# Performance work log

Measured on AMD Instinct MI355X. Metric: run time of the kernel, lower is better.

## Reference

```python
import jax, jax.numpy as jnp
import numpy as np

H = 128          # GRU hidden size (fixed in module)
EPS = 1e-8       # torch CosineSimilarity eps


def _gru_dir(x, w_ih, w_hh, b_ih, b_hh, reverse):
    # x: [B, L, D]; torch GRU gate math, single direction
    B = x.shape[0]
    gx = jnp.einsum('bld,gd->blg', x, w_ih) + b_ih  # [B, L, 3H]

    def step(h, gx_t):
        gh = h @ w_hh.T + b_hh
        xr, xz, xn = jnp.split(gx_t, 3, axis=-1)
        hr, hz, hn = jnp.split(gh, 3, axis=-1)
        r = jax.nn.sigmoid(xr + hr)
        z = jax.nn.sigmoid(xz + hz)
        n = jnp.tanh(xn + r * hn)
        h_new = (1.0 - z) * n + z * h
        return h_new, h_new

    h0 = jnp.zeros((B, H), x.dtype)
    h_last, outs = jax.lax.scan(step, h0, jnp.swapaxes(gx, 0, 1), reverse=reverse)
    return jnp.swapaxes(outs, 0, 1), h_last  # [B, L, H], [B, H]


def _bigru(x, p):
    # p = (w_ih_f, w_hh_f, b_ih_f, b_hh_f, w_ih_b, w_hh_b, b_ih_b, b_hh_b)
    of, hf = _gru_dir(x, p[0], p[1], p[2], p[3], False)
    ob, hb = _gru_dir(x, p[4], p[5], p[6], p[7], True)
    # outs concat = torch bidirectional output; [hf, hb] concat == h_n.transpose(1,0).reshape(B,-1)
    return jnp.concatenate([of, ob], axis=-1), jnp.concatenate([hf, hb], axis=-1)


def _cosnorm(x):
    return x / jnp.maximum(jnp.linalg.norm(x, axis=-1, keepdims=True), EPS)


def _forward(context, options, rnn_p, attn_p):
    ctx_outs, ctx_h = _bigru(context, rnn_p)  # [B, L1, 2H], [B, 2H]

    def per_option(option):  # option: [B, L2, D]
        opt_outs, _ = _bigru(option, rnn_p)  # [B, L2, 2H]
        # cosine-similarity attention == matmul of L2-normalized vectors
        # (replaces the original O(B*L2*L1*2H) repeated tensors, same math)
        att = jnp.einsum('bqh,bkh->bqk', _cosnorm(opt_outs), _cosnorm(ctx_outs))  # [B, L2, L1]
        att = jax.nn.softmax(att, axis=2)  # softmax over context positions (dim=2)
        att_opt = jnp.einsum('bqk,bkh->bqh', att, ctx_outs)  # bmm -> [B, L2, 2H]
        cat = jnp.concatenate([att_opt, opt_outs], axis=-1)  # [B, L2, 4H]
        _, ao_h = _bigru(cat, attn_p)  # [B, 2H]
        num = jnp.sum(ctx_h * ao_h, axis=-1)
        den = jnp.maximum(jnp.linalg.norm(ctx_h, axis=-1), EPS) * \
              jnp.maximum(jnp.linalg.norm(ao_h, axis=-1), EPS)
        return num / den  # [B]

    logits = jax.vmap(per_option)(jnp.swapaxes(options, 0, 1))  # [N, B]
    return jax.nn.softmax(logits.T, axis=1)  # [B, N]


def setup_inputs():
    key = jax.random.key(0)
    ks = jax.random.split(key, 24)
    B, L1, L2, N, D = 64, 512, 50, 10, 300
    inp = {
        'context': jax.random.normal(ks[0], (B, L1, D), jnp.float32),
        'context_lens': jax.random.randint(ks[1], (B,), 1, L1),
        'options': jax.random.normal(ks[2], (B, N, L2, D), jnp.float32),
        'option_lens': jax.random.randint(ks[3], (B, N), 1, L2),
    }
    names = ['rw_ih_f', 'rw_hh_f', 'rb_ih_f', 'rb_hh_f',
             'rw_ih_b', 'rw_hh_b', 'rb_ih_b', 'rb_hh_b',
             'aw_ih_f', 'aw_hh_f', 'ab_ih_f', 'ab_hh_f',
             'aw_ih_b', 'aw_hh_b', 'ab_ih_b', 'ab_hh_b']
    shapes = [(3 * H, D), (3 * H, H), (3 * H,), (3 * H,)] * 2 + \
             [(3 * H, 4 * H), (3 * H, H), (3 * H,), (3 * H,)] * 2
    for i, (n, sh) in enumerate(zip(names, shapes)):
        inp[n] = jax.random.normal(ks[4 + i], sh, jnp.float32) * 0.05
    return inp


def reference(context, context_lens, options, option_lens,
              rw_ih_f, rw_hh_f, rb_ih_f, rb_hh_f,
              rw_ih_b, rw_hh_b, rb_ih_b, rb_hh_b,
              aw_ih_f, aw_hh_f, ab_ih_f, ab_hh_f,
              aw_ih_b, aw_hh_b, ab_ih_b, ab_hh_b):
    rnn_p = (rw_ih_f, rw_hh_f, rb_ih_f, rb_hh_f, rw_ih_b, rw_hh_b, rb_ih_b, rb_hh_b)
    attn_p = (aw_ih_f, aw_hh_f, ab_ih_f, ab_hh_f, aw_ih_b, aw_hh_b, ab_ih_b, ab_hh_b)
    return _forward(context, options, rnn_p, attn_p)
```

## Files before the change

### kernel.cpp

```cpp
#include <hip/hip_runtime.h>
#include <math.h>

#define EPS 1e-8f

typedef _Float16 h2_t __attribute__((ext_vector_type(2)));
typedef _Float16 half8 __attribute__((ext_vector_type(8)));
typedef float f32x4 __attribute__((ext_vector_type(4)));

__device__ __forceinline__ float fsig(float x)  { return 1.0f / (1.0f + __expf(-x)); }
__device__ __forceinline__ float ftanh(float x) { return 1.0f - 2.0f / (1.0f + __expf(2.0f * x)); }

__global__ __launch_bounds__(256) void prep_w_k(
    const float* __restrict__ rwf, const float* __restrict__ rwb,
    const float* __restrict__ awf, const float* __restrict__ awb,
    const float* __restrict__ rbf, const float* __restrict__ rbb,
    const float* __restrict__ abf, const float* __restrict__ abb,
    const float* __restrict__ rhf, const float* __restrict__ rhb,
    const float* __restrict__ ahf, const float* __restrict__ ahb,
    _Float16* __restrict__ wrh, _Float16* __restrict__ wah,
    _Float16* __restrict__ wr16, _Float16* __restrict__ wa16,
    float* __restrict__ br, float* __restrict__ ba)
{
    int idx = blockIdx.x * 256 + threadIdx.x;
    if (idx < 768 * 320) {
        int g = idx / 320, k = idx % 320;
        float v = 0.f;
        if (k < 300) v = (g < 384) ? rwf[g * 300 + k] : rwb[(g - 384) * 300 + k];
        wrh[idx] = (_Float16)v;
    }
    if (idx < 768 * 512) {
        int g = idx / 512, k = idx % 512;
        wah[idx] = (_Float16)((g < 384) ? awf[g * 512 + k] : awb[(g - 384) * 512 + k]);
    }
    if (idx < 2 * 384 * 128) {
        int d = idx / 49152, r = idx % 49152;
        wr16[idx] = (_Float16)(d ? rhb[r] : rhf[r]);
        wa16[idx] = (_Float16)(d ? ahb[r] : ahf[r]);
    }
    if (idx < 768) {
        br[idx] = (idx < 384) ? rbf[idx] : rbb[idx - 384];
        ba[idx] = (idx < 384) ? abf[idx] : abb[idx - 384];
    }
}

__global__ __launch_bounds__(256) void conv_k(
    const float* __restrict__ ctx, const float* __restrict__ opt,
    _Float16* __restrict__ ctxh, _Float16* __restrict__ opth)
{
    int idx = blockIdx.x * 256 + threadIdx.x;
    if (idx < 32768 * 320) {
        int r = idx / 320, k = idx % 320;
        ctxh[idx] = (k < 300) ? (_Float16)ctx[r * 300 + k] : (_Float16)0.f;
    }
    if (idx < 32000 * 320) {
        int r = idx / 320, k = idx % 320;
        opth[idx] = (k < 300) ? (_Float16)opt[r * 300 + k] : (_Float16)0.f;
    }
}

template <bool TRBS, bool SPLITA, bool HASBIAS>
__global__ __launch_bounds__(256, 4) void hgemm_k(
    const _Float16* __restrict__ A, const _Float16* __restrict__ A2,
    const _Float16* __restrict__ B, const float* __restrict__ bias,
    _Float16* __restrict__ C, int M, int N, int K,
    int lda, int ldb, int ldc, long sA, long sB, int bdiv, long sC)
{
    const int jn = blockIdx.x * 64;
    const int im = blockIdx.y * 64;
    const int z  = blockIdx.z;
    const _Float16* Bb = B + (size_t)(z / bdiv) * sB;
    _Float16* Cb = C + (size_t)z * sC;

    __shared__ __align__(16) _Float16 As[64 * 64];
    __shared__ __align__(16) _Float16 Bs[64 * 64];

    const int tid  = threadIdx.x;
    const int arow = tid >> 2;
    const int akof = (tid & 3) * 8;
    const int lane = tid & 63;
    const int wv   = tid >> 6;
    const int wm   = (wv & 1) * 32;
    const int wn   = (wv >> 1) * 32;
    const int fm   = lane & 15;
    const int quad = lane >> 4;

    f32x4 acc[2][2];
#pragma unroll
    for (int a = 0; a < 2; a++)
#pragma unroll
        for (int b = 0; b < 2; b++) acc[a][b] = (f32x4)0.f;

    for (int k0 = 0; k0 < K; k0 += 64) {
        {
            const int row = im + arow;
#pragma unroll
            for (int hh = 0; hh < 2; hh++) {
                half8 av = (half8)(_Float16)0.f;
                const int kg = k0 + akof + 32 * hh;
                if (row < M) {
                    if constexpr (SPLITA) {
                        const _Float16* Ah  = A + (size_t)z * sA;
                        const _Float16* A2h = A2 + (size_t)z * sA;
                        const _Float16* ap = (kg < 256)
                            ? (Ah + (size_t)row * lda + kg)
                            : (A2h + (size_t)row * lda + (kg - 256));
                        av = *(const half8*)ap;
                    } else {
                        av = *(const half8*)(A + (size_t)z * sA + (size_t)row * lda + kg);
                    }
                }
                *(half8*)&As[arow * 64 + akof + 32 * hh] = av;
            }
        }
        if constexpr (!TRBS) {
#pragma unroll
            for (int hh = 0; hh < 2; hh++) {
                half8 bv = *(const half8*)(Bb + (size_t)(jn + arow) * ldb
                                           + k0 + akof + 32 * hh);
                *(half8*)&Bs[arow * 64 + akof + 32 * hh] = bv;
            }
        } else {
            const int kk = tid >> 3, noff = (tid & 7) * 8;
            half8 bv0 = *(const half8*)(Bb + (size_t)(k0 + kk) * ldb + jn + noff);
            half8 bv1 = *(const half8*)(Bb + (size_t)(k0 + kk + 32) * ldb + jn + noff);
#pragma unroll
            for (int e = 0; e < 8; e++) {
                Bs[(noff + e) * 64 + kk]      = bv0[e];
                Bs[(noff + e) * 64 + kk + 32] = bv1[e];
            }
        }
        __syncthreads();

        const _Float16* Asp = As + (wm + fm) * 64 + quad * 8;
        const _Float16* Bsp = Bs + (wn + fm) * 64 + quad * 8;
#pragma unroll
        for (int kh = 0; kh < 64; kh += 32) {
            half8 a0 = *(const half8*)(Asp + kh);
            half8 a1 = *(const half8*)(Asp + 16 * 64 + kh);
            half8 b0 = *(const half8*)(Bsp + kh);
            half8 b1 = *(const half8*)(Bsp + 16 * 64 + kh);
            acc[0][0] = __builtin_amdgcn_mfma_f32_16x16x32_f16(a0, b0, acc[0][0], 0, 0, 0);
            acc[0][1] = __builtin_amdgcn_mfma_f32_16x16x32_f16(a0, b1, acc[0][1], 0, 0, 0);
            acc[1][0] = __builtin_amdgcn_mfma_f32_16x16x32_f16(a1, b0, acc[1][0], 0, 0, 0);
            acc[1][1] = __builtin_amdgcn_mfma_f32_16x16x32_f16(a1, b1, acc[1][1], 0, 0, 0);
        }
        __syncthreads();
    }

#pragma unroll
    for (int tm = 0; tm < 2; tm++) {
#pragma unroll
        for (int tn = 0; tn < 2; tn++) {
            const int col  = jn + wn + tn * 16 + fm;
            const int row0 = im + wm + tm * 16 + quad * 4;
            const float bv = HASBIAS ? bias[col] : 0.f;
#pragma unroll
            for (int r = 0; r < 4; r++) {
                const int row = row0 + r;
                if (row < M)
                    Cb[(size_t)row * ldc + col] = (_Float16)(acc[tm][tn][r] + bv);
            }
        }
    }
}

__global__ __launch_bounds__(512, 2) void gru_rec_k(
    const _Float16* __restrict__ gx,
    const _Float16* __restrict__ whh16,
    const float* __restrict__ bhh_f, const float* __restrict__ bhh_b,
    _Float16* __restrict__ outs_h, float* __restrict__ hfin, int L)
{
    const int dir = blockIdx.x & 1;
    const int s   = blockIdx.x >> 1;
    const int t   = threadIdx.x;
    const int w   = t >> 6;
    const int l   = t & 63;
    const int i   = w * 16 + (l & 15);
    const int kq  = l >> 4;
    const _Float16* Wd = whh16 + (size_t)dir * 49152;
    const float* bh = dir ? bhh_b : bhh_f;

    h2_t w2[3][16];
#pragma unroll
    for (int j = 0; j < 3; j++) {
        const _Float16* Wr = Wd + (size_t)(i + 128 * j) * 128 + 32 * kq;
#pragma unroll
        for (int q = 0; q < 16; q++)
            w2[j][q] = *(const h2_t*)(Wr + 2 * q);
    }
    const float b0 = bh[i], b1 = bh[i + 128], b2 = bh[i + 256];

    __shared__ __align__(16) _Float16 h1[2][128];
    __shared__ __align__(16) _Float16 gxs[64][384];
    __shared__ __align__(16) _Float16 outb[64][128];
    if (t < 128) h1[0][t] = (_Float16)0.f;
    float hprev = 0.f;

    for (int t0 = 0; t0 < L; t0 += 64) {
        const int Tc = (L - t0 < 64) ? (L - t0) : 64;
#pragma unroll
        for (int r = 0; r < 6; r++) {
            const int q = t + 512 * r;
            if (q < Tc * 48) {
                const int j = q / 48, off = (q % 48) * 8;
                const int tt = dir ? (L - 1 - (t0 + j)) : (t0 + j);
                *(half8*)&gxs[j][off] =
                    *(const half8*)(gx + ((size_t)s * L + tt) * 768 + dir * 384 + off);
            }
        }
        __syncthreads();

        for (int j = 0; j < Tc; j++) {
            const int cb = (t0 + j) & 1;
            const h2_t* hp = (const h2_t*)&h1[cb][32 * kq];
            float a0 = 0.f, a1 = 0.f, a2 = 0.f;
#pragma unroll
            for (int q = 0; q < 16; q++) {
                h2_t hq = hp[q];
                a0 = __builtin_amdgcn_fdot2(w2[0][q], hq, a0, false);
                a1 = __builtin_amdgcn_fdot2(w2[1][q], hq, a1, false);
                a2 = __builtin_amdgcn_fdot2(w2[2][q], hq, a2, false);
            }
            a0 += __shfl_xor(a0, 16); a0 += __shfl_xor(a0, 32);
            a1 += __shfl_xor(a1, 16); a1 += __shfl_xor(a1, 32);
            a2 += __shfl_xor(a2, 16); a2 += __shfl_xor(a2, 32);
            const float xc0 = (float)gxs[j][i];
            const float xc1 = (float)gxs[j][i + 128];
            const float xc2 = (float)gxs[j][i + 256];
            const float r  = fsig(xc0 + a0 + b0);
            const float zz = fsig(xc1 + a1 + b1);
            const float n  = ftanh(xc2 + r * (a2 + b2));
            const float hnew = (1.0f - zz) * n + zz * hprev;
            hprev = hnew;
            if (kq == 0) {
                h1[cb ^ 1][i] = (_Float16)hnew;
                outb[j][i]    = (_Float16)hnew;
            }
            __syncthreads();
        }

        if (outs_h) {
#pragma unroll
            for (int r = 0; r < 2; r++) {
                const int q = t + 512 * r;
                if (q < Tc * 16) {
                    const int j = q / 16, off = (q % 16) * 8;
                    const int tt = dir ? (L - 1 - (t0 + j)) : (t0 + j);
                    *(half8*)(outs_h + ((size_t)s * L + tt) * 256 + dir * 128 + off) =
                        *(const half8*)&outb[j][off];
                }
            }
        }
    }
    if (hfin && kq == 0) hfin[(size_t)s * 256 + dir * 128 + i] = hprev;
}

__global__ __launch_bounds__(256) void rowinv_k(const _Float16* __restrict__ x,
                                                float* __restrict__ rinv)
{
    const int row = blockIdx.x;
    float v = (float)x[(size_t)row * 256 + threadIdx.x];
    float ss = v * v;
#pragma unroll
    for (int o = 32; o > 0; o >>= 1) ss += __shfl_down(ss, o);
    __shared__ float ps[4];
    if ((threadIdx.x & 63) == 0) ps[threadIdx.x >> 6] = ss;
    __syncthreads();
    if (threadIdx.x == 0)
        rinv[row] = 1.0f / fmaxf(sqrtf(ps[0] + ps[1] + ps[2] + ps[3]), EPS);
}

__global__ __launch_bounds__(256) void att_softmax_k(
    _Float16* __restrict__ att, const float* __restrict__ rinv_opt_l,
    const float* __restrict__ rinv_ctx, int sbase)
{
    const int row = blockIdx.x;
    const int b = (sbase + row / 50) / 10;
    _Float16* p = att + (size_t)row * 512;
    const float* rc = rinv_ctx + b * 512;
    const float sA = rinv_opt_l[row];
    const int t = threadIdx.x;

    float v0 = (float)p[t]       * (sA * rc[t]);
    float v1 = (float)p[t + 256] * (sA * rc[t + 256]);

    __shared__ float red[4];
    float m = fmaxf(v0, v1);
#pragma unroll
    for (int o = 32; o > 0; o >>= 1) m = fmaxf(m, __shfl_down(m, o));
    if ((t & 63) == 0) red[t >> 6] = m;
    __syncthreads();
    m = fmaxf(fmaxf(red[0], red[1]), fmaxf(red[2], red[3]));
    float e0 = __expf(v0 - m), e1 = __expf(v1 - m);
    float ssum = e0 + e1;
#pragma unroll
    for (int o = 32; o > 0; o >>= 1) ssum += __shfl_down(ssum, o);
    __syncthreads();
    if ((t & 63) == 0) red[t >> 6] = ssum;
    __syncthreads();
    float inv = 1.0f / (red[0] + red[1] + red[2] + red[3]);
    p[t]       = (_Float16)(e0 * inv);
    p[t + 256] = (_Float16)(e1 * inv);
}

__global__ __launch_bounds__(256) void logits_k(const float* __restrict__ ch,
                                                const float* __restrict__ ah,
                                                float* __restrict__ logits)
{
    const int s = blockIdx.x;
    const int b = s / 10;
    const int t = threadIdx.x;
    float a = ch[b * 256 + t];
    float c = ah[(size_t)s * 256 + t];
    float num = a * c, na = a * a, nc = c * c;
#pragma unroll
    for (int o = 32; o > 0; o >>= 1) {
        num += __shfl_down(num, o);
        na  += __shfl_down(na,  o);
        nc  += __shfl_down(nc,  o);
    }
    __shared__ float pn[4], pa[4], pc[4];
    if ((t & 63) == 0) { pn[t >> 6] = num; pa[t >> 6] = na; pc[t >> 6] = nc; }
    __syncthreads();
    if (t == 0) {
        float sn = pn[0] + pn[1] + pn[2] + pn[3];
        float sa = pa[0] + pa[1] + pa[2] + pa[3];
        float sc = pc[0] + pc[1] + pc[2] + pc[3];
        logits[s] = sn / (fmaxf(sqrtf(sa), EPS) * fmaxf(sqrtf(sc), EPS));
    }
}

__global__ __launch_bounds__(64) void soft10_k(const float* __restrict__ logits,
                                               float* __restrict__ out)
{
    const int b = blockIdx.x;
    const int t = threadIdx.x;
    __shared__ float v[10];
    if (t < 10) v[t] = logits[b * 10 + t];
    __syncthreads();
    if (t < 10) {
        float m = v[0];
#pragma unroll
        for (int i = 1; i < 10; i++) m = fmaxf(m, v[i]);
        float ssum = 0.f;
#pragma unroll
        for (int i = 0; i < 10; i++) ssum += __expf(v[i] - m);
        out[b * 10 + t] = __expf(v[t] - m) / ssum;
    }
}

extern "C" void kernel_launch(void* const* d_in, const int* in_sizes, int n_in,
                              void* d_out, int out_size, void* d_ws, size_t ws_size,
                              hipStream_t stream)
{
    const float* context = (const float*)d_in[0];
    const float* options = (const float*)d_in[2];
    const float* rw_ih_f = (const float*)d_in[4];
    const float* rw_hh_f = (const float*)d_in[5];
    const float* rb_ih_f = (const float*)d_in[6];
    const float* rb_hh_f = (const float*)d_in[7];
    const float* rw_ih_b = (const float*)d_in[8];
    const float* rw_hh_b = (const float*)d_in[9];
    const float* rb_ih_b = (const float*)d_in[10];
    const float* rb_hh_b = (const float*)d_in[11];
    const float* aw_ih_f = (const float*)d_in[12];
    const float* aw_hh_f = (const float*)d_in[13];
    const float* ab_ih_f = (const float*)d_in[14];
    const float* ab_hh_f = (const float*)d_in[15];
    const float* aw_ih_b = (const float*)d_in[16];
    const float* aw_hh_b = (const float*)d_in[17];
    const float* ab_ih_b = (const float*)d_in[18];
    const float* ab_hh_b = (const float*)d_in[19];

    const size_t persist = 15222144;
    static const int cands[6][2] = {{1,2},{1,4},{2,4},{2,8},{4,16},{8,16}};
    int CC = 8, OC = 16;
    for (int idx = 0; idx < 6; idx++) {
        size_t bc_ = 64 / cands[idx][0], sc_ = 640 / cands[idx][1];
        size_t p = bc_ * 196608;
        if (sc_ * 32000 > p) p = sc_ * 32000;
        if ((persist + p + 2 * sc_ * 6400) * 4 <= ws_size) {
            CC = cands[idx][0]; OC = cands[idx][1]; break;
        }
    }
    const int bc = 64 / CC;
    const int sc = 640 / OC;
    size_t poolsz = (size_t)bc * 196608;
    if ((size_t)sc * 32000 > poolsz) poolsz = (size_t)sc * 32000;

    float* ws = (float*)d_ws;
    size_t off = 0;
    _Float16* wrh   = (_Float16*)(ws + off); off += 122880;
    float*    br    = ws + off;              off += 768;
    _Float16* wah   = (_Float16*)(ws + off); off += 196608;
    float*    ba    = ws + off;              off += 768;
    _Float16* wr16  = (_Float16*)(ws + off); off += 49152;
    _Float16* wa16  = (_Float16*)(ws + off); off += 49152;
    _Float16* couts = (_Float16*)(ws + off); off += 4194304;
    float*    ctxhf = ws + off;              off += 16384;
    float*    aohf  = ws + off;              off += 163840;
    float*    logits= ws + off;              off += 640;
    float*    rinvc = ws + off;              off += 32768;
    float*    rinvo = ws + off;              off += 32000;
    _Float16* ctxh  = (_Float16*)(ws + off); off += 5242880;
    _Float16* opth  = (_Float16*)(ws + off); off += 5120000;
    _Float16* POOL  = (_Float16*)(ws + off); off += poolsz;
    _Float16* P2H   = (_Float16*)(ws + off); off += (size_t)sc * 6400;
    _Float16* P3H   = (_Float16*)(ws + off); off += (size_t)sc * 6400;
    _Float16* ATT   = POOL + (size_t)sc * 38400;

    prep_w_k<<<1536, 256, 0, stream>>>(rw_ih_f, rw_ih_b, aw_ih_f, aw_ih_b,
                                       rb_ih_f, rb_ih_b, ab_ih_f, ab_ih_b,
                                       rw_hh_f, rw_hh_b, aw_hh_f, aw_hh_b,
                                       wrh, wah, wr16, wa16, br, ba);
    conv_k<<<40960, 256, 0, stream>>>(context, options, ctxh, opth);

    for (int c = 0; c < CC; c++) {
        const int Mc = bc * 512;
        hgemm_k<false, false, true><<<dim3(12, Mc / 64, 1), 256, 0, stream>>>(
            ctxh + (size_t)c * Mc * 320, nullptr, wrh, br, POOL,
            Mc, 768, 320, 320, 320, 768, 0, 0, 1, 0);
        gru_rec_k<<<2 * bc, 512, 0, stream>>>(
            POOL, wr16, rb_hh_f, rb_hh_b,
            couts + (size_t)c * Mc * 256, ctxhf + (size_t)c * bc * 256, 512);
    }

    rowinv_k<<<32768, 256, 0, stream>>>(couts, rinvc);

    for (int o = 0; o < OC; o++) {
        const int base = o * sc;
        const int Mo = sc * 50;
        const _Float16* ctxB = couts + (size_t)(base / 10) * 131072;

        hgemm_k<false, false, true><<<dim3(12, (Mo + 63) / 64, 1), 256, 0, stream>>>(
            opth + (size_t)base * 50 * 320, nullptr, wrh, br, POOL,
            Mo, 768, 320, 320, 320, 768, 0, 0, 1, 0);
        gru_rec_k<<<2 * sc, 512, 0, stream>>>(
            POOL, wr16, rb_hh_f, rb_hh_b, P2H, nullptr, 50);
        rowinv_k<<<Mo, 256, 0, stream>>>(P2H, rinvo + (size_t)base * 50);
        hgemm_k<false, false, false><<<dim3(8, 1, sc), 256, 0, stream>>>(
            P2H, nullptr, ctxB, nullptr, ATT,
            50, 512, 256, 256, 256, 512, 12800, 131072, 10, 25600);
        att_softmax_k<<<Mo, 256, 0, stream>>>(ATT, rinvo + (size_t)base * 50,
                                              rinvc, base);
        hgemm_k<true, false, false><<<dim3(4, 1, sc), 256, 0, stream>>>(
            ATT, nullptr, ctxB, nullptr, P3H,
            50, 256, 512, 512, 256, 256, 25600, 131072, 10, 12800);
        hgemm_k<false, true, true><<<dim3(12, (Mo + 63) / 64, 1), 256, 0, stream>>>(
            P3H, P2H, wah, ba, POOL,
            Mo, 768, 512, 256, 512, 768, 0, 0, 1, 0);
        gru_rec_k<<<2 * sc, 512, 0, stream>>>(
            POOL, wa16, ab_hh_f, ab_hh_b, nullptr, aohf + (size_t)base * 256, 50);
    }

    logits_k<<<640, 256, 0, stream>>>(ctxhf, aohf, logits);
    soft10_k<<<64, 64, 0, stream>>>(logits, (float*)d_out);
}
```

Measured before the change: 1.193 ms.

## Batch 16 sequences per GRU block and compute recurrence with MFMA

Replaces the one-sequence-per-block fdot2 GRU recurrence with a kernel that processes 16 sequences per block and computes the hidden-state matmul using 16x16x32 f16 MFMA, with the weights held in registers. Input-gate values are prefetched one step ahead into registers instead of being staged through shared memory in 64-step chunks. Outputs are written directly to global memory, and the hidden state uses a swizzled shared-memory layout. The aim is to raise matrix throughput per serial step and cut the number of blocks. The trade-off is far fewer blocks, which means lower parallelism for small batches, plus high register pressure.

```diff
diff --git a/kernel.cpp b/kernel.cpp
--- a/kernel.cpp
+++ b/kernel.cpp
@@ -164,95 +164,146 @@
     }
 }
 
-__global__ __launch_bounds__(512, 2) void gru_rec_k(
+#define GRU_STEP(TCUR, CB, CUR, NXT)                                           \
+  {                                                                            \
+    const int tcur_ = (TCUR);                                                  \
+    if (tcur_ + 1 < L) {                                                       \
+      _Pragma("unroll") for (int r = 0; r < 4; r++) {                          \
+        const _Float16* gn = gp[r] + stp;                                      \
+        if (vmask[r]) {                                                        \
+          _Pragma("unroll") for (int p = 0; p < 3; p++)                        \
+            NXT[p][r] = *(const h2_t*)(gn + p * 128);                          \
+        }                                                                      \
+      }                                                                        \
+    }                                                                          \
+    half8 af[4];                                                               \
+    {                                                                          \
+      const char* hb = (const char*)&h1[CB][0];                                \
+      _Pragma("unroll") for (int kf = 0; kf < 4; kf++)                         \
+        af[kf] = *(const half8*)(hb + c * 256 +                                \
+                                 ((kf * 64 + rg * 16) ^ ((c & 7) << 4)));      \
+    }                                                                          \
+    f32x4 acc[3][2];                                                           \
+    _Pragma("unroll") for (int p = 0; p < 3; p++)                              \
+      _Pragma("unroll") for (int u = 0; u < 2; u++)                            \
+        acc[p][u] = (f32x4)0.f;                                                \
+    _Pragma("unroll") for (int kf = 0; kf < 4; kf++)                           \
+      _Pragma("unroll") for (int p = 0; p < 3; p++)                            \
+        _Pragma("unroll") for (int u = 0; u < 2; u++)                          \
+          acc[p][u] = __builtin_amdgcn_mfma_f32_16x16x32_f16(                  \
+              af[kf], wb[p][u][kf], acc[p][u], 0, 0, 0);                       \
+    _Pragma("unroll") for (int r = 0; r < 4; r++) {                            \
+      const float xr0 = (float)CUR[0][r][0], xr1 = (float)CUR[0][r][1];        \
+      const float xz0 = (float)CUR[1][r][0], xz1 = (float)CUR[1][r][1];        \
+      const float xn0 = (float)CUR[2][r][0], xn1 = (float)CUR[2][r][1];        \
+      const float rr0 = fsig(xr0 + acc[0][0][r] + bR0);                        \
+      const float rr1 = fsig(xr1 + acc[0][1][r] + bR1);                        \
+      const float zz0 = fsig(xz0 + acc[1][0][r] + bZ0);                        \
+      const float zz1 = fsig(xz1 + acc[1][1][r] + bZ1);                        \
+      const float nn0 = ftanh(xn0 + rr0 * (acc[2][0][r] + bN0));               \
+      const float nn1 = ftanh(xn1 + rr1 * (acc[2][1][r] + bN1));               \
+      const float h0v = (1.f - zz0) * nn0 + zz0 * hp[r][0];                    \
+      const float h1v = (1.f - zz1) * nn1 + zz1 * hp[r][1];                    \
+      hp[r][0] = h0v; hp[r][1] = h1v;                                          \
+      h2_t hw; hw[0] = (_Float16)h0v; hw[1] = (_Float16)h1v;                   \
+      const int sq = rg * 4 + r;                                               \
+      *(h2_t*)((char*)&h1[(CB) ^ 1][0] + sq * 256 +                            \
+               ((ub * 2) ^ ((sq & 7) << 4))) = hw;                             \
+      if (outs_h && vmask[r]) {                                                \
+        const int tw = dir ? (L - 1 - tcur_) : tcur_;                          \
+        *(h2_t*)(outs_h + ((size_t)(sb + sq) * L + tw) * 256 +                 \
+                 dir * 128 + ub) = hw;                                         \
+      }                                                                        \
+    }                                                                          \
+    _Pragma("unroll") for (int r = 0; r < 4; r++) gp[r] += stp;                \
+    asm volatile("s_waitcnt lgkmcnt(0)" ::: "memory");                         \
+    __builtin_amdgcn_s_barrier();                                              \
+  }
+
+__global__ __launch_bounds__(256, 1) void gru_batch_k(
     const _Float16* __restrict__ gx,
     const _Float16* __restrict__ whh16,
     const float* __restrict__ bhh_f, const float* __restrict__ bhh_b,
-    _Float16* __restrict__ outs_h, float* __restrict__ hfin, int L)
+    _Float16* __restrict__ outs_h,
+    float* __restrict__ hfin,
+    int L, int nseq)
 {
     const int dir = blockIdx.x & 1;
-    const int s   = blockIdx.x >> 1;
+    const int g   = blockIdx.x >> 1;
     const int t   = threadIdx.x;
     const int w   = t >> 6;
     const int l   = t & 63;
-    const int i   = w * 16 + (l & 15);
-    const int kq  = l >> 4;
+    const int c   = l & 15;
+    const int rg  = l >> 4;
+    const int ub  = w * 32 + 2 * c;
+    const int sb  = g * 16;
     const _Float16* Wd = whh16 + (size_t)dir * 49152;
     const float* bh = dir ? bhh_b : bhh_f;
 
-    h2_t w2[3][16];
-#pragma unroll
-    for (int j = 0; j < 3; j++) {
-        const _Float16* Wr = Wd + (size_t)(i + 128 * j) * 128 + 32 * kq;
-#pragma unroll
-        for (int q = 0; q < 16; q++)
-            w2[j][q] = *(const h2_t*)(Wr + 2 * q);
-    }
-    const float b0 = bh[i], b1 = bh[i + 128], b2 = bh[i + 256];
-
-    __shared__ __align__(16) _Float16 h1[2][128];
-    __shared__ __align__(16) _Float16 gxs[64][384];
-    __shared__ __align__(16) _Float16 outb[64][128];
-    if (t < 128) h1[0][t] = (_Float16)0.f;
-    float hprev = 0.f;
-
-    for (int t0 = 0; t0 < L; t0 += 64) {
-        const int Tc = (L - t0 < 64) ? (L - t0) : 64;
-#pragma unroll
-        for (int r = 0; r < 6; r++) {
-            const int q = t + 512 * r;
-            if (q < Tc * 48) {
-                const int j = q / 48, off = (q % 48) * 8;
-                const int tt = dir ? (L - 1 - (t0 + j)) : (t0 + j);
-                *(half8*)&gxs[j][off] =
-                    *(const half8*)(gx + ((size_t)s * L + tt) * 768 + dir * 384 + off);
+    half8 wb[3][2][4];
+#pragma unroll
+    for (int p = 0; p < 3; p++)
+#pragma unroll
+        for (int u = 0; u < 2; u++)
+#pragma unroll
+            for (int kf = 0; kf < 4; kf++)
+                wb[p][u][kf] = *(const half8*)(
+                    Wd + (size_t)(p * 128 + ub + u) * 128 + kf * 32 + rg * 8);
+
+    const float bR0 = bh[ub],       bR1 = bh[ub + 1];
+    const float bZ0 = bh[128 + ub], bZ1 = bh[128 + ub + 1];
+    const float bN0 = bh[256 + ub], bN1 = bh[256 + ub + 1];
+
+    __shared__ __align__(16) _Float16 h1[2][2048];
+    {
+        half8 z = (half8)(_Float16)0.f;
+        *(half8*)&h1[0][t * 8] = z;
+        *(half8*)&h1[1][t * 8] = z;
+    }
+
+    float hp[4][2];
+#pragma unroll
+    for (int r = 0; r < 4; r++) { hp[r][0] = 0.f; hp[r][1] = 0.f; }
+
+    const int tt0 = dir ? (L - 1) : 0;
+    const int stp = dir ? -768 : 768;
+    const _Float16* gp[4];
+    bool vmask[4];
+#pragma unroll
+    for (int r = 0; r < 4; r++) {
+        const int sq = rg * 4 + r;
+        vmask[r] = (sb + sq) < nseq;
+        gp[r] = gx + ((size_t)(sb + sq) * L + tt0) * 768 + dir * 384 + ub;
+    }
+
+    h2_t gA[3][4], gB[3][4];
+#pragma unroll
+    for (int p = 0; p < 3; p++)
+#pragma unroll
+        for (int r = 0; r < 4; r++) {
+            h2_t v = (h2_t)(_Float16)0.f;
+            if (vmask[r]) v = *(const h2_t*)(gp[r] + p * 128);
+            gA[p][r] = v;
+        }
+
+    __syncthreads();
+
+    for (int tc = 0; tc < L; tc += 2) {
+        GRU_STEP(tc,     0, gA, gB);
+        GRU_STEP(tc + 1, 1, gB, gA);
+    }
+
+    if (hfin) {
+#pragma unroll
+        for (int r = 0; r < 4; r++) {
+            const int sq = rg * 4 + r;
+            if (vmask[r]) {
+                float* hf = hfin + (size_t)(sb + sq) * 256 + dir * 128 + ub;
+                hf[0] = hp[r][0];
+                hf[1] = hp[r][1];
             }
         }
-        __syncthreads();
-
-        for (int j = 0; j < Tc; j++) {
-            const int cb = (t0 + j) & 1;
-            const h2_t* hp = (const h2_t*)&h1[cb][32 * kq];
-            float a0 = 0.f, a1 = 0.f, a2 = 0.f;
-#pragma unroll
-            for (int q = 0; q < 16; q++) {
-                h2_t hq = hp[q];
-                a0 = __builtin_amdgcn_fdot2(w2[0][q], hq, a0, false);
-                a1 = __builtin_amdgcn_fdot2(w2[1][q], hq, a1, false);
-                a2 = __builtin_amdgcn_fdot2(w2[2][q], hq, a2, false);
-            }
-            a0 += __shfl_xor(a0, 16); a0 += __shfl_xor(a0, 32);
-            a1 += __shfl_xor(a1, 16); a1 += __shfl_xor(a1, 32);
-            a2 += __shfl_xor(a2, 16); a2 += __shfl_xor(a2, 32);
-            const float xc0 = (float)gxs[j][i];
-            const float xc1 = (float)gxs[j][i + 128];
-            const float xc2 = (float)gxs[j][i + 256];
-            const float r  = fsig(xc0 + a0 + b0);
-            const float zz = fsig(xc1 + a1 + b1);
-            const float n  = ftanh(xc2 + r * (a2 + b2));
-            const float hnew = (1.0f - zz) * n + zz * hprev;
-            hprev = hnew;
-            if (kq == 0) {
-                h1[cb ^ 1][i] = (_Float16)hnew;
-                outb[j][i]    = (_Float16)hnew;
-            }
-            __syncthreads();
-        }
-
-        if (outs_h) {
-#pragma unroll
-            for (int r = 0; r < 2; r++) {
-                const int q = t + 512 * r;
-                if (q < Tc * 16) {
-                    const int j = q / 16, off = (q % 16) * 8;
-                    const int tt = dir ? (L - 1 - (t0 + j)) : (t0 + j);
-                    *(half8*)(outs_h + ((size_t)s * L + tt) * 256 + dir * 128 + off) =
-                        *(const half8*)&outb[j][off];
-                }
-            }
-        }
-    }
-    if (hfin && kq == 0) hfin[(size_t)s * 256 + dir * 128 + i] = hprev;
+    }
 }
 
 __global__ __launch_bounds__(256) void rowinv_k(const _Float16* __restrict__ x,
@@ -420,9 +471,9 @@
         hgemm_k<false, false, true><<<dim3(12, Mc / 64, 1), 256, 0, stream>>>(
             ctxh + (size_t)c * Mc * 320, nullptr, wrh, br, POOL,
             Mc, 768, 320, 320, 320, 768, 0, 0, 1, 0);
-        gru_rec_k<<<2 * bc, 512, 0, stream>>>(
+        gru_batch_k<<<2 * ((bc + 15) / 16), 256, 0, stream>>>(
             POOL, wr16, rb_hh_f, rb_hh_b,
-            couts + (size_t)c * Mc * 256, ctxhf + (size_t)c * bc * 256, 512);
+            couts + (size_t)c * Mc * 256, ctxhf + (size_t)c * bc * 256, 512, bc);
     }
 
     rowinv_k<<<32768, 256, 0, stream>>>(couts, rinvc);
@@ -435,8 +486,8 @@
         hgemm_k<false, false, true><<<dim3(12, (Mo + 63) / 64, 1), 256, 0, stream>>>(
             opth + (size_t)base * 50 * 320, nullptr, wrh, br, POOL,
             Mo, 768, 320, 320, 320, 768, 0, 0, 1, 0);
-        gru_rec_k<<<2 * sc, 512, 0, stream>>>(
-            POOL, wr16, rb_hh_f, rb_hh_b, P2H, nullptr, 50);
+        gru_batch_k<<<2 * ((sc + 15) / 16), 256, 0, stream>>>(
+            POOL, wr16, rb_hh_f, rb_hh_b, P2H, nullptr, 50, sc);
         rowinv_k<<<Mo, 256, 0, stream>>>(P2H, rinvo + (size_t)base * 50);
         hgemm_k<false, false, false><<<dim3(8, 1, sc), 256, 0, stream>>>(
             P2H, nullptr, ctxB, nullptr, ATT,
@@ -449,8 +500,8 @@
         hgemm_k<false, true, true><<<dim3(12, (Mo + 63) / 64, 1), 256, 0, stream>>>(
             P3H, P2H, wah, ba, POOL,
             Mo, 768, 512, 256, 512, 768, 0, 0, 1, 0);
-        gru_rec_k<<<2 * sc, 512, 0, stream>>>(
-            POOL, wa16, ab_hh_f, ab_hh_b, nullptr, aohf + (size_t)base * 256, 50);
+        gru_batch_k<<<2 * ((sc + 15) / 16), 256, 0, stream>>>(
+            POOL, wa16, ab_hh_f, ab_hh_b, nullptr, aohf + (size_t)base * 256, 50, sc);
     }
 
     logits_k<<<640, 256, 0, stream>>>(ctxhf, aohf, logits);
```

Result: slower. 1.592 ms (+33.4%).
